# Kernel optimization log

Measured on AMD Instinct MI355X. Metric: run time of the kernel, lower is better.

Reference implementation:

```python
import jax, jax.numpy as jnp
import numpy as np


def _nearest(img, cy, cx):
    # PyTorch F.grid_sample(mode='nearest', align_corners=False, padding_mode='zeros').
    # img: [B,C,H,W]; cy,cx: [B,N] normalized coords in [-1,1] (cy->H axis, cx->W axis).
    B, C, H, W = img.shape
    iy = jnp.rint((cy + 1.0) * H / 2.0 - 0.5)  # unnormalize then nearbyint
    ix = jnp.rint((cx + 1.0) * W / 2.0 - 0.5)
    valid = (iy >= 0) & (iy < H) & (ix >= 0) & (ix < W)
    flat = (jnp.clip(iy, 0, H - 1).astype(jnp.int32) * W
            + jnp.clip(ix, 0, W - 1).astype(jnp.int32))  # [B,N]
    g = jnp.take_along_axis(img.reshape(B, C, H * W), flat[:, None, :], axis=2)  # [B,C,N]
    g = jnp.where(valid[:, None, :], g, 0.0)
    return g.transpose(0, 2, 1)  # [B,N,C]


def setup_inputs() -> dict:
    key = jax.random.key(0)
    ks = jax.random.split(key, 16)
    B, N = 2, 16384
    h, w = 64, 64       # LR feat / lr_guide resolution
    H, W = 256, 256     # HR guide resolution
    Cf, Cg = 128, 128   # feat_dim, guide_dim
    inp = {
        'feat': jax.random.normal(ks[0], (B, Cf, h, w), jnp.float32),
        'coord': jax.random.uniform(ks[1], (B, N, 2), jnp.float32) * 2.0 - 1.0,
        'hr_guide': jax.random.normal(ks[2], (B, Cg, H, W), jnp.float32),
        'lr_guide': jax.random.normal(ks[3], (B, Cg, h, w), jnp.float32),
    }
    dims = [386, 1024, 512, 256, 128, 2]  # imnet_in_dim -> hidden_list -> out_dim
    for i in range(5):
        fan_in, fan_out = dims[i], dims[i + 1]
        scale = np.sqrt(2.0 / fan_in).astype(np.float32)
        inp[f'W{i}'] = jax.random.normal(ks[4 + i], (fan_out, fan_in), jnp.float32) * scale
        inp[f'b{i}'] = jnp.zeros((fan_out,), jnp.float32)
    return inp


def reference(feat, coord, hr_guide, lr_guide, W0, b0, W1, b1, W2, b2, W3, b3, W4, b4):
    b, c, h, w = feat.shape
    # make_coord((h,w), flatten=False).permute(2,0,1): channel 0 = y (h axis), 1 = x (w axis)
    ys = -1.0 + 2.0 * (jnp.arange(h, dtype=jnp.float32) + 0.5) / h
    xs = -1.0 + 2.0 * (jnp.arange(w, dtype=jnp.float32) + 0.5) / w
    fc = jnp.stack([jnp.broadcast_to(ys[:, None], (h, w)),
                    jnp.broadcast_to(xs[None, :], (h, w))], 0)[None]  # [1,2,h,w]
    fc = jnp.broadcast_to(fc, (b, 2, h, w))

    # coord.flip(-1) as grid -> grid x = coord[...,1] (W axis), grid y = coord[...,0] (H axis)
    q_guide_hr = _nearest(hr_guide, coord[..., 0], coord[..., 1])  # [B,N,Cg]

    # 4 offsets (vx,vy) in [-1,1]x[-1,1], scaled by rx=1/h, ry=1/w (loop order of torch code)
    offs = jnp.array([[-1., -1.], [-1., 1.], [1., -1.], [1., 1.]], jnp.float32)
    offs = offs * jnp.array([1.0 / h, 1.0 / w], jnp.float32)
    cK = coord[None] + offs[:, None, None, :]  # [4,B,N,2]

    samp = jax.vmap(_nearest, in_axes=(None, 0, 0))
    q_feat = samp(feat, cK[..., 0], cK[..., 1])      # [4,B,N,Cf]
    q_coord = samp(fc, cK[..., 0], cK[..., 1])       # [4,B,N,2]
    q_lr = samp(lr_guide, cK[..., 0], cK[..., 1])    # [4,B,N,Cg]

    rel = (coord[None] - q_coord) * jnp.array([float(h), float(w)], jnp.float32)  # [4,B,N,2]
    qg_hr = jnp.broadcast_to(q_guide_hr[None], q_lr.shape)
    inp = jnp.concatenate([q_feat, qg_hr, qg_hr - q_lr, rel], axis=-1)  # [4,B,N,386]

    x = inp
    for Wl, bl in ((W0, b0), (W1, b1), (W2, b2), (W3, b3)):
        x = jax.nn.relu(x @ Wl.T + bl)
    preds = x @ W4.T + b4                      # [4,B,N,2]
    preds = jnp.moveaxis(preds, 0, -1)         # [B,N,2,4]
    wgt = jax.nn.softmax(preds[:, :, 1, :], axis=-1)
    return jnp.sum(preds[:, :, 0, :] * wgt, axis=-1, keepdims=True)  # [B,N,1]
```

## Files before the change

### kernel.cpp

```cpp
#include <hip/hip_runtime.h>
#include <cstdint>

typedef __attribute__((ext_vector_type(8))) _Float16 half8;
typedef __attribute__((ext_vector_type(16))) float   f32x16;

#define BN 2
#define NN 16384
#define FH 64
#define FW 64
#define GH 256
#define GW 256
#define CC 128
#define M_TOTAL (4*BN*NN)
#define MROWS 64
#define NBLK (M_TOTAL/MROWS)

#define SX 424
#define SC 136
#define S2 264
#define S4 136
#define OFF_HC 27136
#define OFF_H3 16896
#define LDS_ELEMS 35840

#define MFMA(a,b,c) __builtin_amdgcn_mfma_f32_32x32x16_f16((a),(b),(c),0,0,0)

static __device__ __forceinline__ f32x16 zero16() {
  f32x16 z;
#pragma unroll
  for (int i = 0; i < 16; ++i) z[i] = 0.f;
  return z;
}
static __device__ __forceinline__ half8 zero8() {
  half8 z;
#pragma unroll
  for (int e = 0; e < 8; ++e) z[e] = (_Float16)0.f;
  return z;
}

__global__ void pack_w(const float* __restrict__ wsrc, _Float16* __restrict__ out,
                       int NT, int K, int KT) {
  int idx = blockIdx.x * 256 + threadIdx.x;
  int total = NT * KT * 64;
  if (idx >= total) return;
  int l = idx & 63;
  int t = idx >> 6;
  int kt = t % KT;
  int jt = t / KT;
  int row = jt * 32 + (l & 31);
  int k0 = kt * 16 + (l >> 5) * 8;
  _Float16* o = out + (size_t)idx * 8;
#pragma unroll
  for (int e = 0; e < 8; ++e) {
    int k = k0 + e;
    float v = (k < K) ? wsrc[(size_t)row * K + k] : 0.f;
    o[e] = (_Float16)v;
  }
}

__global__ void transpose_to_hwc(const float* __restrict__ in, _Float16* __restrict__ out,
                                 int C, int HH, int WW) {
  __shared__ float tile[32][33];
  const int xt = blockIdx.x, ct = blockIdx.y;
  const int bb = blockIdx.z / HH, y = blockIdx.z % HH;
  const int tx = threadIdx.x, ty = threadIdx.y;
  const int x0 = xt * 32, c0 = ct * 32;
#pragma unroll
  for (int i = 0; i < 4; ++i) {
    int c = c0 + ty + i * 8;
    tile[ty + i * 8][tx] = in[((size_t)(bb * C + c) * HH + y) * WW + x0 + tx];
  }
  __syncthreads();
#pragma unroll
  for (int i = 0; i < 4; ++i) {
    int x = x0 + ty + i * 8;
    out[((size_t)(bb * HH + y) * WW + x) * C + c0 + tx] = (_Float16)tile[tx][ty + i * 8];
  }
}

template<bool RELU>
static __device__ __forceinline__ void store_tile(const f32x16 acc, _Float16* lout, int ldo,
                                                  int row0, int col0,
                                                  const float* __restrict__ biasBase, int lane) {
  const int m = row0 + (lane & 31);
  const int s4 = (lane >> 5) * 4;
  _Float16* rp = lout + (size_t)m * ldo + col0 + s4;
  const float* bp = biasBase + s4;
#pragma unroll
  for (int g = 0; g < 4; ++g) {
    float4 bv = *(const float4*)(bp + 8 * g);
    union { _Float16 h[4]; unsigned long long u; } pk;
#pragma unroll
    for (int e = 0; e < 4; ++e) {
      float v = acc[4 * g + e] + ((const float*)&bv)[e];
      if (RELU) v = fmaxf(v, 0.f);
      pk.h[e] = (_Float16)v;
    }
    *(unsigned long long*)(rp + 8 * g) = pk.u;
  }
}

__global__ __launch_bounds__(512, 4) void jiif_main(
    const float* __restrict__ coord,
    const _Float16* __restrict__ featT, const _Float16* __restrict__ hrT,
    const _Float16* __restrict__ lrT,
    const _Float16* __restrict__ W0p, const _Float16* __restrict__ W1p,
    const _Float16* __restrict__ W2p, const _Float16* __restrict__ W3p,
    const float* __restrict__ b0, const float* __restrict__ b1,
    const float* __restrict__ b2, const float* __restrict__ b3,
    const float* __restrict__ W4, const float* __restrict__ b4,
    float* __restrict__ preds) {
  extern __shared__ _Float16 lds[];
  const int tid = threadIdx.x;
  const int w = tid >> 6, lane = tid & 63;
  const int m0 = blockIdx.x * MROWS;
  _Float16* X   = lds;
  _Float16* Hc  = lds + OFF_HC;
  _Float16* H2r = lds;
  _Float16* H3r = lds + OFF_H3;
  _Float16* H4r = lds;

  {
    const int r = tid >> 3;
    const int g = tid & 7;
    const int row = m0 + r;
    const int n = row & (NN - 1);
    const int bb = (row >> 14) & (BN - 1);
    const int k = row >> 15;
    const float c0 = coord[((size_t)bb * NN + n) * 2 + 0];
    const float c1 = coord[((size_t)bb * NN + n) * 2 + 1];
    const float cy = c0 + ((k < 2) ? -1.f : 1.f) * (1.f / FH);
    const float cx = c1 + ((k & 1) ? 1.f : -1.f) * (1.f / FW);
    const float fy = rintf((cy + 1.f) * (FH * 0.5f) - 0.5f);
    const float fx = rintf((cx + 1.f) * (FW * 0.5f) - 0.5f);
    const bool vF = (fy >= 0.f) && (fy < (float)FH) && (fx >= 0.f) && (fx < (float)FW);
    const int iy = max(0, min(FH - 1, (int)fy));
    const int ix = max(0, min(FW - 1, (int)fx));
    const float gy = rintf((c0 + 1.f) * (GH * 0.5f) - 0.5f);
    const float gx = rintf((c1 + 1.f) * (GW * 0.5f) - 0.5f);
    const bool vH = (gy >= 0.f) && (gy < (float)GH) && (gx >= 0.f) && (gx < (float)GW);
    const int jy = max(0, min(GH - 1, (int)gy));
    const int jx = max(0, min(GW - 1, (int)gx));
    const _Float16* fp = featT + (size_t)((bb * FH + iy) * FW + ix) * CC;
    const _Float16* lp = lrT  + (size_t)((bb * FH + iy) * FW + ix) * CC;
    const _Float16* hp = hrT  + (size_t)((bb * GH + jy) * GW + jx) * CC;
    _Float16* xr = X + (size_t)r * SX;
#pragma unroll
    for (int t = 0; t < 2; ++t) {
      const int c8 = g * 16 + t * 8;
      half8 fv = vF ? *(const half8*)(fp + c8) : zero8();
      half8 lv = vF ? *(const half8*)(lp + c8) : zero8();
      half8 hv = vH ? *(const half8*)(hp + c8) : zero8();
      *(half8*)(xr + c8) = fv;
      *(half8*)(xr + CC + c8) = hv;
      half8 dv = hv - lv;
      *(half8*)(xr + 2 * CC + c8) = dv;
    }
    if (g == 0) {
      const float qc0 = vF ? (-1.f + (float)(2 * iy + 1) * (1.f / FH)) : 0.f;
      const float qc1 = vF ? (-1.f + (float)(2 * ix + 1) * (1.f / FW)) : 0.f;
      xr[384] = (_Float16)((c0 - qc0) * (float)FH);
      xr[385] = (_Float16)((c1 - qc1) * (float)FW);
#pragma unroll
      for (int c = 386; c < 416; ++c) xr[c] = (_Float16)0.f;
    }
  }
  __syncthreads();

  const int m31 = lane & 31;
  const int s8 = (lane >> 5) * 8;
  const int mt = w & 1;
  const int jl = w >> 1;

  f32x16 a2_00 = zero16(), a2_01 = zero16(), a2_10 = zero16(), a2_11 = zero16();
#pragma unroll 1
  for (int c = 0; c < 8; ++c) {
    f32x16 a0 = zero16();
    {
      const _Float16* xb = X + (size_t)(mt * 32 + m31) * SX + s8;
      const _Float16* wb = W0p + ((size_t)((c * 4 + jl) * 26) * 64 + lane) * 8;
#pragma unroll 2
      for (int kt = 0; kt < 26; ++kt) {
        half8 A = *(const half8*)(wb + kt * 512);
        half8 B = *(const half8*)(xb + kt * 16);
        a0 = MFMA(A, B, a0);
      }
    }
    store_tile<true>(a0, Hc, SC, mt * 32, jl * 32, b0 + c * 128 + jl * 32, lane);
    __syncthreads();
    {
      const _Float16* hb0 = Hc + (size_t)m31 * SC + s8;
      const _Float16* hb1 = Hc + (size_t)(32 + m31) * SC + s8;
      const _Float16* w1a = W1p + ((size_t)(w * 64 + c * 8) * 64 + lane) * 8;
      const _Float16* w1b = W1p + ((size_t)((w + 8) * 64 + c * 8) * 64 + lane) * 8;
#pragma unroll 2
      for (int kt = 0; kt < 8; ++kt) {
        half8 A0 = *(const half8*)(w1a + kt * 512);
        half8 A1 = *(const half8*)(w1b + kt * 512);
        half8 B0 = *(const half8*)(hb0 + kt * 16);
        half8 B1 = *(const half8*)(hb1 + kt * 16);
        a2_00 = MFMA(A0, B0, a2_00);
        a2_01 = MFMA(A0, B1, a2_01);
        a2_10 = MFMA(A1, B0, a2_10);
        a2_11 = MFMA(A1, B1, a2_11);
      }
    }
    __syncthreads();
  }

  f32x16 a3a = zero16(), a3b = zero16();
  const int j2a = w >> 1, j2b = (w >> 1) + 4;
  store_tile<true>(a2_00, H2r, S2, 0,  w * 32, b1 + w * 32, lane);
  store_tile<true>(a2_01, H2r, S2, 32, w * 32, b1 + w * 32, lane);
  __syncthreads();
  {
    const _Float16* hb = H2r + (size_t)(mt * 32 + m31) * S2 + s8;
    const _Float16* wa = W2p + ((size_t)(j2a * 32) * 64 + lane) * 8;
    const _Float16* wb2 = W2p + ((size_t)(j2b * 32) * 64 + lane) * 8;
#pragma unroll 2
    for (int kt = 0; kt < 16; ++kt) {
      half8 A0 = *(const half8*)(wa + kt * 512);
      half8 A1 = *(const half8*)(wb2 + kt * 512);
      half8 B = *(const half8*)(hb + kt * 16);
      a3a = MFMA(A0, B, a3a);
      a3b = MFMA(A1, B, a3b);
    }
  }
  __syncthreads();
  store_tile<true>(a2_10, H2r, S2, 0,  w * 32, b1 + 256 + w * 32, lane);
  store_tile<true>(a2_11, H2r, S2, 32, w * 32, b1 + 256 + w * 32, lane);
  __syncthreads();
  {
    const _Float16* hb = H2r + (size_t)(mt * 32 + m31) * S2 + s8;
    const _Float16* wa = W2p + ((size_t)(j2a * 32 + 16) * 64 + lane) * 8;
    const _Float16* wb2 = W2p + ((size_t)(j2b * 32 + 16) * 64 + lane) * 8;
#pragma unroll 2
    for (int kt = 0; kt < 16; ++kt) {
      half8 A0 = *(const half8*)(wa + kt * 512);
      half8 A1 = *(const half8*)(wb2 + kt * 512);
      half8 B = *(const half8*)(hb + kt * 16);
      a3a = MFMA(A0, B, a3a);
      a3b = MFMA(A1, B, a3b);
    }
  }
  store_tile<true>(a3a, H3r, S2, mt * 32, j2a * 32, b2 + j2a * 32, lane);
  store_tile<true>(a3b, H3r, S2, mt * 32, j2b * 32, b2 + j2b * 32, lane);
  __syncthreads();

  {
    const int j3 = w >> 1;
    f32x16 a4 = zero16();
    const _Float16* hb = H3r + (size_t)(mt * 32 + m31) * S2 + s8;
    const _Float16* wb3 = W3p + ((size_t)(j3 * 16) * 64 + lane) * 8;
#pragma unroll 2
    for (int kt = 0; kt < 16; ++kt) {
      half8 A = *(const half8*)(wb3 + kt * 512);
      half8 B = *(const half8*)(hb + kt * 16);
      a4 = MFMA(A, B, a4);
    }
    store_tile<true>(a4, H4r, S4, mt * 32, j3 * 32, b3 + j3 * 32, lane);
  }
  __syncthreads();

  {
    const int m = tid >> 3;
    const int sub = tid & 7;
    const int j = sub & 1;
    const int q = sub >> 1;
    const _Float16* h4 = H4r + (size_t)m * S4 + q * 32;
    const float* w4 = W4 + j * CC + q * 32;
    float s = 0.f;
#pragma unroll
    for (int cc = 0; cc < 32; ++cc) s += (float)h4[cc] * w4[cc];
    s += __shfl_xor(s, 2);
    s += __shfl_xor(s, 4);
    if (q == 0) preds[(size_t)(m0 + m) * 2 + j] = s + b4[j];
  }
}

__global__ void jiif_combine(const float* __restrict__ preds, float* __restrict__ out) {
  const int i = blockIdx.x * 256 + threadIdx.x;
  if (i >= BN * NN) return;
  float p0[4], p1[4];
#pragma unroll
  for (int k = 0; k < 4; ++k) {
    p0[k] = preds[((size_t)k * BN * NN + i) * 2 + 0];
    p1[k] = preds[((size_t)k * BN * NN + i) * 2 + 1];
  }
  float mx = fmaxf(fmaxf(p1[0], p1[1]), fmaxf(p1[2], p1[3]));
  float se = 0.f, so = 0.f;
#pragma unroll
  for (int k = 0; k < 4; ++k) {
    float e = expf(p1[k] - mx);
    se += e;
    so += p0[k] * e;
  }
  out[i] = so / se;
}

extern "C" void kernel_launch(void* const* d_in, const int* in_sizes, int n_in,
                              void* d_out, int out_size, void* d_ws, size_t ws_size,
                              hipStream_t stream) {
  const float* feat  = (const float*)d_in[0];
  const float* coord = (const float*)d_in[1];
  const float* hr    = (const float*)d_in[2];
  const float* lr    = (const float*)d_in[3];
  const float* W0 = (const float*)d_in[4];  const float* b0 = (const float*)d_in[5];
  const float* W1 = (const float*)d_in[6];  const float* b1 = (const float*)d_in[7];
  const float* W2 = (const float*)d_in[8];  const float* b2 = (const float*)d_in[9];
  const float* W3 = (const float*)d_in[10]; const float* b3 = (const float*)d_in[11];
  const float* W4 = (const float*)d_in[12]; const float* b4 = (const float*)d_in[13];

  char* ws = (char*)d_ws;
  _Float16* W0p   = (_Float16*)(ws + 0);
  _Float16* W1p   = (_Float16*)(ws + 851968);
  _Float16* W2p   = (_Float16*)(ws + 1900544);
  _Float16* W3p   = (_Float16*)(ws + 2162688);
  _Float16* featT = (_Float16*)(ws + 2228224);
  _Float16* hrT   = (_Float16*)(ws + 4325376);
  _Float16* lrT   = (_Float16*)(ws + 37879808);
  float* preds    = (float*)(ws + 39976960);
  if (ws_size < 41025536) return;

  pack_w<<<208, 256, 0, stream>>>(W0, W0p, 32, 386, 26);
  pack_w<<<256, 256, 0, stream>>>(W1, W1p, 16, 1024, 64);
  pack_w<<<64,  256, 0, stream>>>(W2, W2p, 8, 512, 32);
  pack_w<<<16,  256, 0, stream>>>(W3, W3p, 4, 256, 16);

  transpose_to_hwc<<<dim3(2, 4, 128), dim3(32, 8), 0, stream>>>(feat, featT, CC, FH, FW);
  transpose_to_hwc<<<dim3(8, 4, 512), dim3(32, 8), 0, stream>>>(hr,   hrT,   CC, GH, GW);
  transpose_to_hwc<<<dim3(2, 4, 128), dim3(32, 8), 0, stream>>>(lr,   lrT,   CC, FH, FW);

  (void)hipFuncSetAttribute((const void*)jiif_main,
                            hipFuncAttributeMaxDynamicSharedMemorySize, LDS_ELEMS * 2);
  jiif_main<<<NBLK, 512, LDS_ELEMS * 2, stream>>>(
      coord, featT, hrT, lrT, W0p, W1p, W2p, W3p, b0, b1, b2, b3, W4, b4, preds);

  jiif_combine<<<(BN * NN + 255) / 256, 256, 0, stream>>>(preds, (float*)d_out);
}
```

Measured before the change: 377.3 us.

## Widen per-wave MLP tiles to cover both row halves and batch-load fragments

Each wave now computes both 32-row halves for its output columns, so every weight fragment is reused twice. Layer 0 and 1 are chunked into 4 steps of 256 hidden units instead of 8 of 128, and layer 2 keeps all 512 inputs in LDS so the extra barrier pass goes away. The MFMA loops load batches of fragments into registers before issuing MFMAs under raised s_setprio, and W0 is padded to 28 k-tiles. This costs more LDS and registers, with launch bounds dropping from 4 to 2 blocks per CU, which lowers occupancy.

```diff
diff --git a/kernel.cpp b/kernel.cpp
--- a/kernel.cpp
+++ b/kernel.cpp
@@ -15,13 +15,14 @@
 #define MROWS 64
 #define NBLK (M_TOTAL/MROWS)
 
-#define SX 424
-#define SC 136
-#define S2 264
-#define S4 136
-#define OFF_HC 27136
-#define OFF_H3 16896
-#define LDS_ELEMS 35840
+#define SX  456
+#define SC  264
+#define S2H 520
+#define S3  264
+#define S4  136
+#define OFF_HC 29184
+#define OFF_H3 33280
+#define LDS_ELEMS 50176
 
 #define MFMA(a,b,c) __builtin_amdgcn_mfma_f32_32x32x16_f16((a),(b),(c),0,0,0)
 
@@ -100,7 +101,7 @@
   }
 }
 
-__global__ __launch_bounds__(512, 4) void jiif_main(
+__global__ __launch_bounds__(512, 2) void jiif_main(
     const float* __restrict__ coord,
     const _Float16* __restrict__ featT, const _Float16* __restrict__ hrT,
     const _Float16* __restrict__ lrT,
@@ -156,109 +157,134 @@
       half8 dv = hv - lv;
       *(half8*)(xr + 2 * CC + c8) = dv;
     }
+    *(unsigned long long*)(xr + 384 + g * 8) = 0ull;
+    *(unsigned long long*)(xr + 384 + g * 8 + 4) = 0ull;
     if (g == 0) {
       const float qc0 = vF ? (-1.f + (float)(2 * iy + 1) * (1.f / FH)) : 0.f;
       const float qc1 = vF ? (-1.f + (float)(2 * ix + 1) * (1.f / FW)) : 0.f;
       xr[384] = (_Float16)((c0 - qc0) * (float)FH);
       xr[385] = (_Float16)((c1 - qc1) * (float)FW);
-#pragma unroll
-      for (int c = 386; c < 416; ++c) xr[c] = (_Float16)0.f;
     }
   }
   __syncthreads();
 
   const int m31 = lane & 31;
   const int s8 = (lane >> 5) * 8;
-  const int mt = w & 1;
-  const int jl = w >> 1;
+  const _Float16* xb0 = X + (size_t)m31 * SX + s8;
+  const _Float16* xb1 = X + (size_t)(32 + m31) * SX + s8;
 
   f32x16 a2_00 = zero16(), a2_01 = zero16(), a2_10 = zero16(), a2_11 = zero16();
 #pragma unroll 1
-  for (int c = 0; c < 8; ++c) {
-    f32x16 a0 = zero16();
+  for (int c = 0; c < 4; ++c) {
+    f32x16 a0lo = zero16(), a0hi = zero16();
     {
-      const _Float16* xb = X + (size_t)(mt * 32 + m31) * SX + s8;
-      const _Float16* wb = W0p + ((size_t)((c * 4 + jl) * 26) * 64 + lane) * 8;
-#pragma unroll 2
-      for (int kt = 0; kt < 26; ++kt) {
-        half8 A = *(const half8*)(wb + kt * 512);
-        half8 B = *(const half8*)(xb + kt * 16);
-        a0 = MFMA(A, B, a0);
-      }
-    }
-    store_tile<true>(a0, Hc, SC, mt * 32, jl * 32, b0 + c * 128 + jl * 32, lane);
+      const _Float16* wb = W0p + ((size_t)(c * 8 + w) * 28 * 64 + lane) * 8;
+#pragma unroll 1
+      for (int t = 0; t < 4; ++t) {
+        half8 A[7], B0[7], B1[7];
+#pragma unroll
+        for (int i = 0; i < 7; ++i) {
+          const int kt = t * 7 + i;
+          A[i]  = *(const half8*)(wb + kt * 512);
+          B0[i] = *(const half8*)(xb0 + kt * 16);
+          B1[i] = *(const half8*)(xb1 + kt * 16);
+        }
+        __builtin_amdgcn_s_setprio(1);
+#pragma unroll
+        for (int i = 0; i < 7; ++i) {
+          a0lo = MFMA(A[i], B0[i], a0lo);
+          a0hi = MFMA(A[i], B1[i], a0hi);
+        }
+        __builtin_amdgcn_s_setprio(0);
+      }
+    }
+    store_tile<true>(a0lo, Hc, SC, 0,  w * 32, b0 + c * 256 + w * 32, lane);
+    store_tile<true>(a0hi, Hc, SC, 32, w * 32, b0 + c * 256 + w * 32, lane);
     __syncthreads();
     {
+      const _Float16* w1a = W1p + ((size_t)(w * 64 + c * 16) * 64 + lane) * 8;
+      const _Float16* w1b = W1p + ((size_t)((w + 8) * 64 + c * 16) * 64 + lane) * 8;
       const _Float16* hb0 = Hc + (size_t)m31 * SC + s8;
       const _Float16* hb1 = Hc + (size_t)(32 + m31) * SC + s8;
-      const _Float16* w1a = W1p + ((size_t)(w * 64 + c * 8) * 64 + lane) * 8;
-      const _Float16* w1b = W1p + ((size_t)((w + 8) * 64 + c * 8) * 64 + lane) * 8;
-#pragma unroll 2
-      for (int kt = 0; kt < 8; ++kt) {
-        half8 A0 = *(const half8*)(w1a + kt * 512);
-        half8 A1 = *(const half8*)(w1b + kt * 512);
-        half8 B0 = *(const half8*)(hb0 + kt * 16);
-        half8 B1 = *(const half8*)(hb1 + kt * 16);
-        a2_00 = MFMA(A0, B0, a2_00);
-        a2_01 = MFMA(A0, B1, a2_01);
-        a2_10 = MFMA(A1, B0, a2_10);
-        a2_11 = MFMA(A1, B1, a2_11);
+#pragma unroll 1
+      for (int t = 0; t < 4; ++t) {
+        half8 A0[4], A1[4], B0[4], B1[4];
+#pragma unroll
+        for (int i = 0; i < 4; ++i) {
+          const int kt = t * 4 + i;
+          A0[i] = *(const half8*)(w1a + kt * 512);
+          A1[i] = *(const half8*)(w1b + kt * 512);
+          B0[i] = *(const half8*)(hb0 + kt * 16);
+          B1[i] = *(const half8*)(hb1 + kt * 16);
+        }
+        __builtin_amdgcn_s_setprio(1);
+#pragma unroll
+        for (int i = 0; i < 4; ++i) {
+          a2_00 = MFMA(A0[i], B0[i], a2_00);
+          a2_01 = MFMA(A0[i], B1[i], a2_01);
+          a2_10 = MFMA(A1[i], B0[i], a2_10);
+          a2_11 = MFMA(A1[i], B1[i], a2_11);
+        }
+        __builtin_amdgcn_s_setprio(0);
       }
     }
     __syncthreads();
   }
 
-  f32x16 a3a = zero16(), a3b = zero16();
-  const int j2a = w >> 1, j2b = (w >> 1) + 4;
-  store_tile<true>(a2_00, H2r, S2, 0,  w * 32, b1 + w * 32, lane);
-  store_tile<true>(a2_01, H2r, S2, 32, w * 32, b1 + w * 32, lane);
-  __syncthreads();
+  store_tile<true>(a2_00, H2r, S2H, 0,  w * 32,       b1 + w * 32,       lane);
+  store_tile<true>(a2_01, H2r, S2H, 32, w * 32,       b1 + w * 32,       lane);
+  store_tile<true>(a2_10, H2r, S2H, 0,  256 + w * 32, b1 + 256 + w * 32, lane);
+  store_tile<true>(a2_11, H2r, S2H, 32, 256 + w * 32, b1 + 256 + w * 32, lane);
+  __syncthreads();
+
   {
-    const _Float16* hb = H2r + (size_t)(mt * 32 + m31) * S2 + s8;
-    const _Float16* wa = W2p + ((size_t)(j2a * 32) * 64 + lane) * 8;
-    const _Float16* wb2 = W2p + ((size_t)(j2b * 32) * 64 + lane) * 8;
-#pragma unroll 2
-    for (int kt = 0; kt < 16; ++kt) {
-      half8 A0 = *(const half8*)(wa + kt * 512);
-      half8 A1 = *(const half8*)(wb2 + kt * 512);
-      half8 B = *(const half8*)(hb + kt * 16);
-      a3a = MFMA(A0, B, a3a);
-      a3b = MFMA(A1, B, a3b);
-    }
-  }
-  __syncthreads();
-  store_tile<true>(a2_10, H2r, S2, 0,  w * 32, b1 + 256 + w * 32, lane);
-  store_tile<true>(a2_11, H2r, S2, 32, w * 32, b1 + 256 + w * 32, lane);
-  __syncthreads();
+    f32x16 a3lo = zero16(), a3hi = zero16();
+    const _Float16* wb = W2p + ((size_t)(w * 32) * 64 + lane) * 8;
+    const _Float16* hb0 = H2r + (size_t)m31 * S2H + s8;
+    const _Float16* hb1 = H2r + (size_t)(32 + m31) * S2H + s8;
+#pragma unroll 1
+    for (int t = 0; t < 4; ++t) {
+      half8 A[8], B0[8], B1[8];
+#pragma unroll
+      for (int i = 0; i < 8; ++i) {
+        const int kt = t * 8 + i;
+        A[i]  = *(const half8*)(wb + kt * 512);
+        B0[i] = *(const half8*)(hb0 + kt * 16);
+        B1[i] = *(const half8*)(hb1 + kt * 16);
+      }
+      __builtin_amdgcn_s_setprio(1);
+#pragma unroll
+      for (int i = 0; i < 8; ++i) {
+        a3lo = MFMA(A[i], B0[i], a3lo);
+        a3hi = MFMA(A[i], B1[i], a3hi);
+      }
+      __builtin_amdgcn_s_setprio(0);
+    }
+    store_tile<true>(a3lo, H3r, S3, 0,  w * 32, b2 + w * 32, lane);
+    store_tile<true>(a3hi, H3r, S3, 32, w * 32, b2 + w * 32, lane);
+  }
+  __syncthreads();
+
   {
-    const _Float16* hb = H2r + (size_t)(mt * 32 + m31) * S2 + s8;
-    const _Float16* wa = W2p + ((size_t)(j2a * 32 + 16) * 64 + lane) * 8;
-    const _Float16* wb2 = W2p + ((size_t)(j2b * 32 + 16) * 64 + lane) * 8;
-#pragma unroll 2
-    for (int kt = 0; kt < 16; ++kt) {
-      half8 A0 = *(const half8*)(wa + kt * 512);
-      half8 A1 = *(const half8*)(wb2 + kt * 512);
-      half8 B = *(const half8*)(hb + kt * 16);
-      a3a = MFMA(A0, B, a3a);
-      a3b = MFMA(A1, B, a3b);
-    }
-  }
-  store_tile<true>(a3a, H3r, S2, mt * 32, j2a * 32, b2 + j2a * 32, lane);
-  store_tile<true>(a3b, H3r, S2, mt * 32, j2b * 32, b2 + j2b * 32, lane);
-  __syncthreads();
-
-  {
-    const int j3 = w >> 1;
+    const int j3 = w & 3, mts = w >> 2;
     f32x16 a4 = zero16();
-    const _Float16* hb = H3r + (size_t)(mt * 32 + m31) * S2 + s8;
-    const _Float16* wb3 = W3p + ((size_t)(j3 * 16) * 64 + lane) * 8;
-#pragma unroll 2
-    for (int kt = 0; kt < 16; ++kt) {
-      half8 A = *(const half8*)(wb3 + kt * 512);
-      half8 B = *(const half8*)(hb + kt * 16);
-      a4 = MFMA(A, B, a4);
-    }
-    store_tile<true>(a4, H4r, S4, mt * 32, j3 * 32, b3 + j3 * 32, lane);
+    const _Float16* wb = W3p + ((size_t)(j3 * 16) * 64 + lane) * 8;
+    const _Float16* hb = H3r + (size_t)(mts * 32 + m31) * S3 + s8;
+#pragma unroll 1
+    for (int t = 0; t < 2; ++t) {
+      half8 A[8], B[8];
+#pragma unroll
+      for (int i = 0; i < 8; ++i) {
+        const int kt = t * 8 + i;
+        A[i] = *(const half8*)(wb + kt * 512);
+        B[i] = *(const half8*)(hb + kt * 16);
+      }
+      __builtin_amdgcn_s_setprio(1);
+#pragma unroll
+      for (int i = 0; i < 8; ++i) a4 = MFMA(A[i], B[i], a4);
+      __builtin_amdgcn_s_setprio(0);
+    }
+    store_tile<true>(a4, H4r, S4, mts * 32, j3 * 32, b3 + j3 * 32, lane);
   }
   __syncthreads();
 
@@ -313,16 +339,16 @@
 
   char* ws = (char*)d_ws;
   _Float16* W0p   = (_Float16*)(ws + 0);
-  _Float16* W1p   = (_Float16*)(ws + 851968);
-  _Float16* W2p   = (_Float16*)(ws + 1900544);
-  _Float16* W3p   = (_Float16*)(ws + 2162688);
-  _Float16* featT = (_Float16*)(ws + 2228224);
-  _Float16* hrT   = (_Float16*)(ws + 4325376);
-  _Float16* lrT   = (_Float16*)(ws + 37879808);
-  float* preds    = (float*)(ws + 39976960);
-  if (ws_size < 41025536) return;
-
-  pack_w<<<208, 256, 0, stream>>>(W0, W0p, 32, 386, 26);
+  _Float16* W1p   = (_Float16*)(ws + 917504);
+  _Float16* W2p   = (_Float16*)(ws + 1966080);
+  _Float16* W3p   = (_Float16*)(ws + 2228224);
+  _Float16* featT = (_Float16*)(ws + 2293760);
+  _Float16* hrT   = (_Float16*)(ws + 4390912);
+  _Float16* lrT   = (_Float16*)(ws + 37945344);
+  float* preds    = (float*)(ws + 40042496);
+  if (ws_size < 41091072) return;
+
+  pack_w<<<224, 256, 0, stream>>>(W0, W0p, 32, 386, 28);
   pack_w<<<256, 256, 0, stream>>>(W1, W1p, 16, 1024, 64);
   pack_w<<<64,  256, 0, stream>>>(W2, W2p, 8, 512, 32);
   pack_w<<<16,  256, 0, stream>>>(W3, W3p, 4, 256, 16);
```

New measurement: 373.1 us. About the same (-1.1%).
